# Optimization experiments

Measured on AMD Instinct MI355X. Metric: run time of the kernel, lower is better.

Reference implementation:

```python
import jax, jax.numpy as jnp
import numpy as np
from jax import lax

CONF_THRES = 0.5
IOU_THRES = 0.45
TOP_K = 2048  # fixed candidate cap for jit-friendly NMS


def _xywh2xyxy(x):
    # x: [N,4] center-x, center-y, w, h -> x1,y1,x2,y2
    xy, wh = x[:, :2], x[:, 2:4]
    return jnp.concatenate([xy - wh / 2, xy + wh / 2], axis=-1)


def _box_iou(b1, b2):
    # b1: [N,4], b2: [M,4] in xyxy -> [N,M]
    area1 = (b1[:, 2] - b1[:, 0]) * (b1[:, 3] - b1[:, 1])
    area2 = (b2[:, 2] - b2[:, 0]) * (b2[:, 3] - b2[:, 1])
    lt = jnp.maximum(b1[:, None, :2], b2[None, :, :2])
    rb = jnp.minimum(b1[:, None, 2:], b2[None, :, 2:])
    inter = jnp.clip(rb - lt, 0).prod(-1)
    return inter / (area1[:, None] + area2[None, :] - inter)


def _nms_per_image(x):
    # x: [N,16] = xywh(4), obj(1), landmarks(10), cls_score(1); nc=1 path
    obj = x[:, 4]
    conf = x[:, 15] * obj          # x[:,15:] *= x[:,4:5], then max over 1 class
    box = _xywh2xyxy(x[:, :4])
    valid = (obj > CONF_THRES) & (conf > CONF_THRES)
    score = jnp.where(valid, conf, -jnp.inf)

    topv, topi = lax.top_k(score, TOP_K)          # sorted descending
    valid_k = jnp.isfinite(topv)                  # [K]
    boxes_k = box[topi]                           # [K,4]; class offset c = 0 (nc=1)
    x_k = x[topi]                                 # [K,16]
    conf_k = conf[topi]

    iou = _box_iou(boxes_k, boxes_k)              # [K,K]

    def body(keep, inp):
        i, iou_row, v = inp
        suppressed = jnp.any(keep & (iou_row > IOU_THRES))
        keep_i = v & ~suppressed
        return keep.at[i].set(keep_i), keep_i

    keep, _ = lax.scan(body, jnp.zeros(TOP_K, bool),
                       (jnp.arange(TOP_K), iou, valid_k))

    # detection row: [x1,y1,x2,y2, conf, 10 landmarks, class(=0)]
    det = jnp.concatenate(
        [boxes_k, conf_k[:, None], x_k[:, 5:15],
         jnp.zeros((TOP_K, 1), x.dtype)], axis=1)
    return jnp.where(keep[:, None], det, jnp.zeros((), x.dtype))


def setup_inputs() -> dict:
    key = jax.random.key(0)
    prediction = jax.random.uniform(key, (8, 100800, 16), dtype=jnp.float32)
    return {"prediction": prediction}


def reference(prediction):
    # prediction: [B, N, 16] -> padded detections [B, TOP_K, 16]
    return jax.vmap(_nms_per_image)(prediction)
```

## Files before the change

kernel.cpp:

```cpp
#include <hip/hip_runtime.h>
#include <stdint.h>

#define NA    100800
#define NIMG  8
#define TOPK  2048
#define NBLK1 99
typedef unsigned long long u64;

__global__ __launch_bounds__(256) void k1_scan(const float* __restrict__ pred,
                                               unsigned* __restrict__ cand32,
                                               int* __restrict__ hist_blocks) {
    __shared__ int lhist[64];
    int t = threadIdx.x;
    int m = blockIdx.y;
    if (t < 64) lhist[t] = 0;
    __syncthreads();
    const float4* p4 = reinterpret_cast<const float4*>(pred + (size_t)m * NA * 16);
    int row0blk = blockIdx.x * 1024;
    for (int pass = 0; pass < 4; ++pass) {
        int row0 = row0blk + pass * 256;
        int i1 = row0 * 4 + 2 * t + 1;
        int i2 = i1 + 512;
        float4 A = make_float4(0.f, 0.f, 0.f, 0.f);
        float4 B = make_float4(0.f, 0.f, 0.f, 0.f);
        if ((i1 >> 2) < NA) A = p4[i1];
        if ((i2 >> 2) < NA) B = p4[i2];
        float aw = __shfl_xor(A.w, 1);
        float bw = __shfl_xor(B.w, 1);
        if (!(t & 1)) {
            int rA = row0 + (t >> 1);
            int rB = rA + 128;
            {
                float obj = A.x, x15 = aw;
                if (rA < NA) {
                    float conf = __fmul_rn(x15, obj);
                    unsigned cb = 0u;
                    if (obj > 0.5f && conf > 0.5f) {
                        cb = __float_as_uint(conf);
                        atomicAdd(&lhist[min(63, (int)((cb - 0x3F000000u) >> 17))], 1);
                    }
                    cand32[(size_t)m * NA + rA] = cb;
                }
            }
            {
                float obj = B.x, x15 = bw;
                if (rB < NA) {
                    float conf = __fmul_rn(x15, obj);
                    unsigned cb = 0u;
                    if (obj > 0.5f && conf > 0.5f) {
                        cb = __float_as_uint(conf);
                        atomicAdd(&lhist[min(63, (int)((cb - 0x3F000000u) >> 17))], 1);
                    }
                    cand32[(size_t)m * NA + rB] = cb;
                }
            }
        }
    }
    __syncthreads();
    if (t < 64) hist_blocks[((size_t)m * NBLK1 + blockIdx.x) * 64 + t] = lhist[t];
}

__global__ void k2a_cutoff(const int* __restrict__ hist_blocks, int* __restrict__ cut,
                           int* __restrict__ pos) {
    int m = blockIdx.x;
    int lane = threadIdx.x;
    int h = 0;
    #pragma unroll 4
    for (int b = 0; b < NBLK1; ++b)
        h += hist_blocks[((size_t)m * NBLK1 + b) * 64 + lane];
    #pragma unroll
    for (int off = 1; off < 64; off <<= 1) {
        int src = lane + off;
        int v = __shfl(h, src < 64 ? src : lane);
        h += (src < 64) ? v : 0;
    }
    int total  = __shfl(h, 0);
    int needed = min(total, TOPK);
    u64 bal = __ballot(h >= needed);
    int cutoff = 63 - __clzll(bal);
    if (lane == 0) { cut[m] = cutoff; pos[m] = 0; }
}

__global__ __launch_bounds__(1024) void k2b_compact(const unsigned* __restrict__ cand32,
                                                    const int* __restrict__ cut,
                                                    u64* __restrict__ comp,
                                                    int* __restrict__ pos) {
    __shared__ int wbase[16];
    __shared__ int sbase;
    int m = blockIdx.y;
    int i = blockIdx.x * 1024 + threadIdx.x;
    int lane = threadIdx.x & 63, wid = threadIdx.x >> 6;
    unsigned cb = (i < NA) ? cand32[(size_t)m * NA + i] : 0u;
    int c = cut[m];
    bool keep = false;
    if (cb) keep = min(63, (int)((cb - 0x3F000000u) >> 17)) >= c;
    u64 bal = __ballot(keep);
    int cnt = __popcll(bal);
    if (lane == 0) wbase[wid] = cnt;
    __syncthreads();
    if (threadIdx.x == 0) {
        int s = 0;
        #pragma unroll
        for (int w = 0; w < 16; ++w) { int v = wbase[w]; wbase[w] = s; s += v; }
        sbase = s ? atomicAdd(&pos[m], s) : 0;
    }
    __syncthreads();
    if (keep) {
        int p = sbase + wbase[wid] + (int)__popcll(bal & ((1ull << lane) - 1ull));
        if (p < 4096)
            comp[(size_t)m * 4096 + p] = ((u64)cb << 32) | (u64)(0xFFFFFFFFu - (unsigned)i);
    }
}

__global__ __launch_bounds__(1024) void k2c_rank(const u64* __restrict__ comp,
                                                 const int* __restrict__ pos,
                                                 const float* __restrict__ pred,
                                                 u64* __restrict__ sel,
                                                 float4* __restrict__ boxes) {
    __shared__ int fcnt[4096];
    __shared__ int fstart[4096];
    __shared__ u64 outb[4096];
    __shared__ int wsum[16];
    int m = blockIdx.x, t = threadIdx.x;
    int M = min(pos[m], 4096);
    const u64* c = comp + (size_t)m * 4096;
    #pragma unroll
    for (int r = 0; r < 4; ++r) { fcnt[t + r * 1024] = 0; outb[t + r * 1024] = 0ull; }
    __syncthreads();
    u64 kk[4]; int rb[4];
    #pragma unroll
    for (int r = 0; r < 4; ++r) {
        int i = t + r * 1024;
        kk[r] = 0ull; rb[r] = -1;
        if (i < M) {
            kk[r] = c[i];
            rb[r] = 4095 - (int)(((unsigned)(kk[r] >> 32) - 0x3F000000u) >> 11);
            atomicAdd(&fcnt[rb[r]], 1);
        }
    }
    __syncthreads();
    int c0 = fcnt[4 * t], c1 = fcnt[4 * t + 1], c2 = fcnt[4 * t + 2], c3 = fcnt[4 * t + 3];
    int s = c0 + c1 + c2 + c3;
    int lane = t & 63, w = t >> 6;
    int incl = s;
    #pragma unroll
    for (int off = 1; off < 64; off <<= 1) {
        int v = __shfl_up(incl, off);
        if (lane >= off) incl += v;
    }
    if (lane == 63) wsum[w] = incl;
    __syncthreads();
    if (w == 0) {
        int v = (lane < 16) ? wsum[lane] : 0;
        #pragma unroll
        for (int off = 1; off < 16; off <<= 1) {
            int u = __shfl_up(v, off);
            if (lane >= off) v += u;
        }
        if (lane < 16) wsum[lane] = v;
    }
    __syncthreads();
    int base = (w > 0 ? wsum[w - 1] : 0) + (incl - s);
    fstart[4 * t]     = base;
    fstart[4 * t + 1] = base + c0;
    fstart[4 * t + 2] = base + c0 + c1;
    fstart[4 * t + 3] = base + c0 + c1 + c2;
    __syncthreads();
    #pragma unroll
    for (int r = 0; r < 4; ++r) {
        if (rb[r] >= 0) {
            int old = atomicSub(&fcnt[rb[r]], 1);
            int slot = fstart[rb[r]] + old - 1;
            outb[slot] = kk[r];
        }
    }
    __syncthreads();
    #pragma unroll
    for (int r = 0; r < 4; ++r) {
        int b = t + r * 1024;
        int st = fstart[b];
        int en = (b < 4095) ? fstart[b + 1] : M;
        for (int x = st + 1; x < en; ++x) {
            u64 key = outb[x];
            int y = x - 1;
            while (y >= st && outb[y] < key) { outb[y + 1] = outb[y]; --y; }
            outb[y + 1] = key;
        }
    }
    __syncthreads();
    #pragma unroll
    for (int r = 0; r < 2; ++r) {
        int i = t + r * 1024;
        u64 key = outb[i];
        sel[(size_t)m * TOPK + i] = key;
        float4 b = make_float4(0.f, 0.f, 0.f, 0.f);
        if (key) {
            unsigned idx = 0xFFFFFFFFu - (unsigned)(key & 0xFFFFFFFFull);
            const float4* rv = reinterpret_cast<const float4*>(pred + ((size_t)m * NA + idx) * 16);
            float4 v = rv[0];
            float hw = __fmul_rn(v.z, 0.5f), hh = __fmul_rn(v.w, 0.5f);
            b.x = __fsub_rn(v.x, hw);
            b.y = __fsub_rn(v.y, hh);
            b.z = __fadd_rn(v.x, hw);
            b.w = __fadd_rn(v.y, hh);
        }
        boxes[(size_t)m * TOPK + i] = b;
    }
}

__global__ __launch_bounds__(1024) void k4_masks(const float4* __restrict__ boxes,
                                                 u64* __restrict__ maskT) {
    __shared__ float4 bx[TOPK];
    int m   = blockIdx.y;
    int grp = blockIdx.x;
    for (int i = threadIdx.x; i < TOPK; i += 1024)
        bx[i] = boxes[(size_t)m * TOPK + i];
    __syncthreads();

    int il = threadIdx.x & 31;
    int w  = threadIdx.x >> 5;
    int i  = grp * 32 + il;
    float4 b1 = bx[i];
    float a1 = __fmul_rn(__fsub_rn(b1.z, b1.x), __fsub_rn(b1.w, b1.y));
    u64 bits = 0ull;
    #pragma unroll 4
    for (int jj = 0; jj < 64; ++jj) {
        float4 b2 = bx[w * 64 + jj];
        float a2 = __fmul_rn(__fsub_rn(b2.z, b2.x), __fsub_rn(b2.w, b2.y));
        float iw = fmaxf(__fsub_rn(fminf(b1.z, b2.z), fmaxf(b1.x, b2.x)), 0.f);
        float ih = fmaxf(__fsub_rn(fminf(b1.w, b2.w), fmaxf(b1.y, b2.y)), 0.f);
        float inter = __fmul_rn(iw, ih);
        float uni   = __fsub_rn(__fadd_rn(a1, a2), inter);
        float iou   = __fdiv_rn(inter, uni);
        if (iou > 0.45f) bits |= (1ull << jj);
    }
    maskT[((size_t)m * 32 + w) * 2048 + i] = bits;
}

__global__ __launch_bounds__(1024) void k5_nms(const u64* __restrict__ sel,
                                               const u64* __restrict__ maskT,
                                               const float* __restrict__ pred,
                                               float4* __restrict__ out) {
    __shared__ u64 remv[32];
    __shared__ u64 kbshare[2];
    __shared__ u64 kws[32];
    int m = blockIdx.x;
    int t = threadIdx.x;
    int lane = t & 63;
    int wv = t >> 6;
    const u64* mt = maskT + (size_t)m * 32 * 2048;
    if (t < 32) remv[t] = 0ull;
    u64 dval = 0ull, sval = 0ull, tval = 0ull;
    u64 cfmask = 0ull;
    u64 mybit = 1ull << lane;
    u64 lowmask = mybit - 1ull;
    if (wv == 0) {
        dval = mt[(size_t)0 * 2048 + lane];
        sval = sel[(size_t)m * TOPK + lane];
        tval = mt[(size_t)0 * 2048 + 64 + lane];
    }
    __syncthreads();

    u64 uA1 = 0ull, uA2 = 0ull, uB1 = 0ull, uB2 = 0ull;

#define K5_SCAN(B) do {                                                       \
    u64 dn = 0ull, sn = 0ull, tn = 0ull;                                      \
    if ((B) < 31) {                                                           \
        int r = ((B) + 1) * 64 + lane;                                        \
        dn = mt[(size_t)((B) + 1) * 2048 + r];                                \
        sn = sel[(size_t)m * TOPK + r];                                       \
        if ((B) < 30) tn = mt[(size_t)((B) + 1) * 2048 + r + 64];             \
    }                                                                         \
    u64 ext = remv[(B)];                                                      \
    u64 validw = __ballot(sval != 0ull);                                      \
    u64 alive = validw & ~ext & ~cfmask;                                      \
    u64 kb = 0ull;                                                            \
    while (alive) {                                                           \
        u64 c = dval & alive & lowmask;                                       \
        u64 ready = __ballot(((alive & mybit) != 0ull) && (c == 0ull));       \
        kb |= ready;                                                          \
        u64 removed = __ballot((dval & ready) != 0ull);                       \
        alive &= ~(ready | removed);                                          \
    }                                                                         \
    cfmask = ((B) < 31) ? __ballot((tval & kb) != 0ull) : 0ull;               \
    if (lane == 0) { kbshare[(B) & 1] = kb; kws[(B)] = kb; }                  \
    dval = dn; sval = sn; tval = tn;                                          \
} while (0)

#define K5_UP_ISSUE(V1, V2, S) do {           \
    int w1_ = (S) + wv, w2_ = (S) + 15 + wv;                                  \
    V1 = (w1_ < 32) ? mt[(size_t)((S) - 1) * 2048 + w1_ * 64 + lane] : 0ull;  \
    V2 = (w2_ < 32) ? mt[(size_t)((S) - 1) * 2048 + w2_ * 64 + lane] : 0ull;  \
} while (0)

#define K5_UP_CONSUME(V1, V2, B) do {                                         \
    u64 kb = kbshare[((B) - 1) & 1];                                          \
    int w1_ = (B) + wv, w2_ = (B) + 15 + wv;                                  \
    u64 c1 = __ballot((V1 & kb) != 0ull);                                     \
    u64 c2 = __ballot((V2 & kb) != 0ull);                                     \
    if (w1_ < 32 && lane == 0) remv[w1_] |= c1;                               \
    if (w2_ < 32 && lane == 0) remv[w2_] |= c2;                               \
} while (0)

    #pragma unroll 1
    for (int it = 0; it < 16; ++it) {
        int b0 = 2 * it, b1 = b0 + 1;
        if (wv == 0) {
            K5_SCAN(b0);
        } else {
            K5_UP_ISSUE(uB1, uB2, b0 + 1);
            if (b0 >= 1) K5_UP_CONSUME(uA1, uA2, b0);
        }
        __syncthreads();
        if (wv == 0) {
            K5_SCAN(b1);
        } else {
            if (b1 + 1 < 32) K5_UP_ISSUE(uA1, uA2, b1 + 1);
            K5_UP_CONSUME(uB1, uB2, b1);
        }
        __syncthreads();
    }
#undef K5_SCAN
#undef K5_UP_ISSUE
#undef K5_UP_CONSUME

    const u64* sl = sel + (size_t)m * TOPK;
    float4* om = out + (size_t)m * TOPK * 4;
    #pragma unroll
    for (int q = t; q < TOPK * 4; q += 1024) {
        int c4 = q & 3;
        int r  = q >> 2;
        float4 o = make_float4(0.f, 0.f, 0.f, 0.f);
        if ((kws[r >> 6] >> (r & 63)) & 1ull) {
            u64 key = sl[r];
            unsigned idx = 0xFFFFFFFFu - (unsigned)(key & 0xFFFFFFFFull);
            const float4* rv = reinterpret_cast<const float4*>(pred + ((size_t)m * NA + idx) * 16);
            float4 v = rv[c4];
            if (c4 == 0) {
                float hw = __fmul_rn(v.z, 0.5f), hh = __fmul_rn(v.w, 0.5f);
                o = make_float4(__fsub_rn(v.x, hw), __fsub_rn(v.y, hh),
                                __fadd_rn(v.x, hw), __fadd_rn(v.y, hh));
            } else if (c4 == 1) {
                o = make_float4(__uint_as_float((unsigned)(key >> 32)), v.y, v.z, v.w);
            } else if (c4 == 2) {
                o = v;
            } else {
                o = make_float4(v.x, v.y, v.z, 0.f);
            }
        }
        om[q] = o;
    }
}

extern "C" void kernel_launch(void* const* d_in, const int* in_sizes, int n_in,
                              void* d_out, int out_size, void* d_ws, size_t ws_size,
                              hipStream_t stream) {
    (void)in_sizes; (void)n_in; (void)out_size; (void)ws_size;
    const float* pred = (const float*)d_in[0];
    char* ws = (char*)d_ws;
    unsigned* cand32   = (unsigned*)(ws + 0);
    u64*      comp     = (u64*)     (ws + 3225600);
    u64*      sel      = (u64*)     (ws + 3487744);
    float4*   boxes    = (float4*)  (ws + 3618816);
    u64*      maskT    = (u64*)     (ws + 3880960);
    int*      histb    = (int*)     (ws + 8075264);
    int*      pos      = (int*)     (ws + 8278016);
    int*      cut      = (int*)     (ws + 8278048);
    float4*   out      = (float4*)d_out;

    hipLaunchKernelGGL(k1_scan,    dim3(NBLK1, NIMG),            dim3(256),  0, stream, pred, cand32, histb);
    hipLaunchKernelGGL(k2a_cutoff, dim3(NIMG),                   dim3(64),   0, stream, histb, cut, pos);
    hipLaunchKernelGGL(k2b_compact,dim3(NBLK1, NIMG),            dim3(1024), 0, stream, cand32, cut, comp, pos);
    hipLaunchKernelGGL(k2c_rank,   dim3(NIMG),                   dim3(1024), 0, stream, comp, pos, pred, sel, boxes);
    hipLaunchKernelGGL(k4_masks,   dim3(64, NIMG),               dim3(1024), 0, stream, boxes, maskT);
    hipLaunchKernelGGL(k5_nms,     dim3(NIMG),                   dim3(1024), 0, stream, sel, maskT, pred, out);
}
```

Before: 98.13 us.

## Compact candidates in scan kernel and fold cutoff/compaction into rank kernel

```diff
diff --git a/kernel.cpp b/kernel.cpp
--- a/kernel.cpp
+++ b/kernel.cpp
@@ -8,12 +8,17 @@
 typedef unsigned long long u64;
 
 __global__ __launch_bounds__(256) void k1_scan(const float* __restrict__ pred,
-                                               unsigned* __restrict__ cand32,
-                                               int* __restrict__ hist_blocks) {
+                                               u64* __restrict__ cand,
+                                               int* __restrict__ hist,
+                                               int* __restrict__ cnt) {
     __shared__ int lhist[64];
+    __shared__ u64 lkeys[1024];
+    __shared__ int lcnt;
+    __shared__ int gbase;
     int t = threadIdx.x;
     int m = blockIdx.y;
     if (t < 64) lhist[t] = 0;
+    if (t == 0) lcnt = 0;
     __syncthreads();
     const float4* p4 = reinterpret_cast<const float4*>(pred + (size_t)m * NA * 16);
     int row0blk = blockIdx.x * 1024;
@@ -34,106 +39,97 @@
                 float obj = A.x, x15 = aw;
                 if (rA < NA) {
                     float conf = __fmul_rn(x15, obj);
-                    unsigned cb = 0u;
                     if (obj > 0.5f && conf > 0.5f) {
-                        cb = __float_as_uint(conf);
+                        unsigned cb = __float_as_uint(conf);
                         atomicAdd(&lhist[min(63, (int)((cb - 0x3F000000u) >> 17))], 1);
+                        int p = atomicAdd(&lcnt, 1);
+                        lkeys[p] = ((u64)cb << 32) | (u64)(0xFFFFFFFFu - (unsigned)rA);
                     }
-                    cand32[(size_t)m * NA + rA] = cb;
                 }
             }
             {
                 float obj = B.x, x15 = bw;
                 if (rB < NA) {
                     float conf = __fmul_rn(x15, obj);
-                    unsigned cb = 0u;
                     if (obj > 0.5f && conf > 0.5f) {
-                        cb = __float_as_uint(conf);
+                        unsigned cb = __float_as_uint(conf);
                         atomicAdd(&lhist[min(63, (int)((cb - 0x3F000000u) >> 17))], 1);
+                        int p = atomicAdd(&lcnt, 1);
+                        lkeys[p] = ((u64)cb << 32) | (u64)(0xFFFFFFFFu - (unsigned)rB);
                     }
-                    cand32[(size_t)m * NA + rB] = cb;
                 }
             }
         }
     }
     __syncthreads();
-    if (t < 64) hist_blocks[((size_t)m * NBLK1 + blockIdx.x) * 64 + t] = lhist[t];
-}
-
-__global__ void k2a_cutoff(const int* __restrict__ hist_blocks, int* __restrict__ cut,
-                           int* __restrict__ pos) {
-    int m = blockIdx.x;
-    int lane = threadIdx.x;
-    int h = 0;
-    #pragma unroll 4
-    for (int b = 0; b < NBLK1; ++b)
-        h += hist_blocks[((size_t)m * NBLK1 + b) * 64 + lane];
-    #pragma unroll
-    for (int off = 1; off < 64; off <<= 1) {
-        int src = lane + off;
-        int v = __shfl(h, src < 64 ? src : lane);
-        h += (src < 64) ? v : 0;
-    }
-    int total  = __shfl(h, 0);
-    int needed = min(total, TOPK);
-    u64 bal = __ballot(h >= needed);
-    int cutoff = 63 - __clzll(bal);
-    if (lane == 0) { cut[m] = cutoff; pos[m] = 0; }
-}
-
-__global__ __launch_bounds__(1024) void k2b_compact(const unsigned* __restrict__ cand32,
-                                                    const int* __restrict__ cut,
-                                                    u64* __restrict__ comp,
-                                                    int* __restrict__ pos) {
-    __shared__ int wbase[16];
-    __shared__ int sbase;
-    int m = blockIdx.y;
-    int i = blockIdx.x * 1024 + threadIdx.x;
-    int lane = threadIdx.x & 63, wid = threadIdx.x >> 6;
-    unsigned cb = (i < NA) ? cand32[(size_t)m * NA + i] : 0u;
-    int c = cut[m];
-    bool keep = false;
-    if (cb) keep = min(63, (int)((cb - 0x3F000000u) >> 17)) >= c;
-    u64 bal = __ballot(keep);
-    int cnt = __popcll(bal);
-    if (lane == 0) wbase[wid] = cnt;
-    __syncthreads();
-    if (threadIdx.x == 0) {
-        int s = 0;
-        #pragma unroll
-        for (int w = 0; w < 16; ++w) { int v = wbase[w]; wbase[w] = s; s += v; }
-        sbase = s ? atomicAdd(&pos[m], s) : 0;
-    }
-    __syncthreads();
-    if (keep) {
-        int p = sbase + wbase[wid] + (int)__popcll(bal & ((1ull << lane) - 1ull));
-        if (p < 4096)
-            comp[(size_t)m * 4096 + p] = ((u64)cb << 32) | (u64)(0xFFFFFFFFu - (unsigned)i);
-    }
-}
-
-__global__ __launch_bounds__(1024) void k2c_rank(const u64* __restrict__ comp,
-                                                 const int* __restrict__ pos,
-                                                 const float* __restrict__ pred,
-                                                 u64* __restrict__ sel,
-                                                 float4* __restrict__ boxes) {
+    if (t < 64 && lhist[t]) atomicAdd(&hist[(m << 6) + t], lhist[t]);
+    if (t == 0) gbase = lcnt ? atomicAdd(&cnt[m], lcnt) : 0;
+    __syncthreads();
+    int n = lcnt;
+    u64* cm = cand + (size_t)m * NA;
+    for (int i = t; i < n; i += 256) cm[gbase + i] = lkeys[i];
+}
+
+__global__ __launch_bounds__(1024) void k2_rank(const u64* __restrict__ cand,
+                                                const int* __restrict__ hist,
+                                                const int* __restrict__ cnt,
+                                                const float* __restrict__ pred,
+                                                u64* __restrict__ sel,
+                                                float4* __restrict__ boxes) {
     __shared__ int fcnt[4096];
     __shared__ int fstart[4096];
     __shared__ u64 outb[4096];
     __shared__ int wsum[16];
+    __shared__ int cutsh, msh;
     int m = blockIdx.x, t = threadIdx.x;
-    int M = min(pos[m], 4096);
-    const u64* c = comp + (size_t)m * 4096;
+    int lane = t & 63, w = t >> 6;
+    if (t == 0) msh = 0;
     #pragma unroll
     for (int r = 0; r < 4; ++r) { fcnt[t + r * 1024] = 0; outb[t + r * 1024] = 0ull; }
     __syncthreads();
+    if (w == 0) {
+        int h = hist[(m << 6) + lane];
+        #pragma unroll
+        for (int off = 1; off < 64; off <<= 1) {
+            int src = lane + off;
+            int v = __shfl(h, src < 64 ? src : lane);
+            h += (src < 64) ? v : 0;
+        }
+        int total  = __shfl(h, 0);
+        int needed = min(total, TOPK);
+        u64 bal = __ballot(h >= needed);
+        int cutoff = 63 - __clzll(bal);
+        if (lane == 0) cutsh = cutoff;
+    }
+    __syncthreads();
+    int cut = cutsh;
+    int count = cnt[m];
+    const u64* cm = cand + (size_t)m * NA;
+    for (int i = t; i < count; i += 1024) {
+        u64 key = cm[i];
+        unsigned cb = (unsigned)(key >> 32);
+        bool keep = min(63, (int)((cb - 0x3F000000u) >> 17)) >= cut;
+        u64 bal = __ballot(keep);
+        if (bal) {
+            int n = __popcll(bal);
+            int base = 0;
+            if (lane == 0) base = atomicAdd(&msh, n);
+            base = __shfl(base, 0);
+            if (keep) {
+                int p = base + (int)__popcll(bal & ((1ull << lane) - 1ull));
+                if (p < 4096) outb[p] = key;
+            }
+        }
+    }
+    __syncthreads();
+    int M = min(msh, 4096);
     u64 kk[4]; int rb[4];
     #pragma unroll
     for (int r = 0; r < 4; ++r) {
         int i = t + r * 1024;
         kk[r] = 0ull; rb[r] = -1;
         if (i < M) {
-            kk[r] = c[i];
+            kk[r] = outb[i];
             rb[r] = 4095 - (int)(((unsigned)(kk[r] >> 32) - 0x3F000000u) >> 11);
             atomicAdd(&fcnt[rb[r]], 1);
         }
@@ -141,7 +137,6 @@
     __syncthreads();
     int c0 = fcnt[4 * t], c1 = fcnt[4 * t + 1], c2 = fcnt[4 * t + 2], c3 = fcnt[4 * t + 3];
     int s = c0 + c1 + c2 + c3;
-    int lane = t & 63, w = t >> 6;
     int incl = s;
     #pragma unroll
     for (int off = 1; off < 64; off <<= 1) {
@@ -358,20 +353,17 @@
     (void)in_sizes; (void)n_in; (void)out_size; (void)ws_size;
     const float* pred = (const float*)d_in[0];
     char* ws = (char*)d_ws;
-    unsigned* cand32   = (unsigned*)(ws + 0);
-    u64*      comp     = (u64*)     (ws + 3225600);
-    u64*      sel      = (u64*)     (ws + 3487744);
-    float4*   boxes    = (float4*)  (ws + 3618816);
-    u64*      maskT    = (u64*)     (ws + 3880960);
-    int*      histb    = (int*)     (ws + 8075264);
-    int*      pos      = (int*)     (ws + 8278016);
-    int*      cut      = (int*)     (ws + 8278048);
+    u64*      cand     = (u64*)     (ws + 0);
+    u64*      sel      = (u64*)     (ws + 6451200);
+    float4*   boxes    = (float4*)  (ws + 6582272);
+    u64*      maskT    = (u64*)     (ws + 6844416);
+    int*      hist     = (int*)     (ws + 11038720);
+    int*      cnt      = (int*)     (ws + 11040768);
     float4*   out      = (float4*)d_out;
 
-    hipLaunchKernelGGL(k1_scan,    dim3(NBLK1, NIMG),            dim3(256),  0, stream, pred, cand32, histb);
-    hipLaunchKernelGGL(k2a_cutoff, dim3(NIMG),                   dim3(64),   0, stream, histb, cut, pos);
-    hipLaunchKernelGGL(k2b_compact,dim3(NBLK1, NIMG),            dim3(1024), 0, stream, cand32, cut, comp, pos);
-    hipLaunchKernelGGL(k2c_rank,   dim3(NIMG),                   dim3(1024), 0, stream, comp, pos, pred, sel, boxes);
-    hipLaunchKernelGGL(k4_masks,   dim3(64, NIMG),               dim3(1024), 0, stream, boxes, maskT);
-    hipLaunchKernelGGL(k5_nms,     dim3(NIMG),                   dim3(1024), 0, stream, sel, maskT, pred, out);
-}
+    hipMemsetAsync(hist, 0, 2048 + 32, stream);
+    hipLaunchKernelGGL(k1_scan,  dim3(NBLK1, NIMG), dim3(256),  0, stream, pred, cand, hist, cnt);
+    hipLaunchKernelGGL(k2_rank,  dim3(NIMG),        dim3(1024), 0, stream, cand, hist, cnt, pred, sel, boxes);
+    hipLaunchKernelGGL(k4_masks, dim3(64, NIMG),    dim3(1024), 0, stream, boxes, maskT);
+    hipLaunchKernelGGL(k5_nms,   dim3(NIMG),        dim3(1024), 0, stream, sel, maskT, pred, out);
+}
```

After: 94.61 us (median of 3 runs). 1.04x faster.
